# Performance work log

Measured on AMD Instinct MI355X. Metric: run time of the kernel, lower is better.

The kernel has to match this reference:

```python
import jax, jax.numpy as jnp
import numpy as np

B, S, D, H, E = 4, 4096, 1024, 16, 8
HID = 4 * D


def _ln(x, g, b, eps=1e-5):
    m = x.mean(-1, keepdims=True)
    v = ((x - m) ** 2).mean(-1, keepdims=True)
    return (x - m) / jnp.sqrt(v + eps) * g + b


def setup_inputs() -> dict:
    key = jax.random.key(0)
    ks = jax.random.split(key, 18)
    s = 0.02
    return {
        "x": jax.random.normal(ks[0], (B, S, D), jnp.float32),
        "conv_w": jax.random.normal(ks[1], (D, D, 3), jnp.float32) * s,
        "conv_b": jnp.zeros((D,), jnp.float32),
        "in_proj_w": jax.random.normal(ks[2], (3 * D, D), jnp.float32) * s,
        "in_proj_b": jnp.zeros((3 * D,), jnp.float32),
        "out_proj_w": jax.random.normal(ks[3], (D, D), jnp.float32) * s,
        "out_proj_b": jnp.zeros((D,), jnp.float32),
        "ln1_g": jnp.ones((D,), jnp.float32),
        "ln1_b": jnp.zeros((D,), jnp.float32),
        "gate_w": jax.random.normal(ks[4], (D, E), jnp.float32) * s,
        "gate_b": jnp.zeros((E,), jnp.float32),
        "w1": jax.random.normal(ks[5], (E, D, HID), jnp.float32) * s,
        "b1": jnp.zeros((E, HID), jnp.float32),
        "w2": jax.random.normal(ks[6], (E, HID, D), jnp.float32) * s,
        "b2": jnp.zeros((E, D), jnp.float32),
        "ln2_g": jnp.ones((D,), jnp.float32),
        "ln2_b": jnp.zeros((D,), jnp.float32),
    }


def reference(x, conv_w, conv_b, in_proj_w, in_proj_b, out_proj_w, out_proj_b,
              ln1_g, ln1_b, gate_w, gate_b, w1, b1, w2, b2, ln2_g, ln2_b):
    b, s, d = x.shape
    h = H
    hd = d // h
    e = w1.shape[0]
    # --- Conv1d over seq axis (kernel 3, padding 1) ---
    xc = jnp.transpose(x, (0, 2, 1))  # (B, D, S)
    xc = jax.lax.conv_general_dilated(
        xc, conv_w, (1,), [(1, 1)], dimension_numbers=("NCH", "OIH", "NCH"))
    x = jnp.transpose(xc + conv_b[None, :, None], (0, 2, 1))  # (B, S, D)
    # --- MultiheadAttention. Faithful to original: batch_first=False, so
    # axis 0 (size B) is treated as the sequence axis, axis 1 (size S) as batch.
    qkv = x @ in_proj_w.T + in_proj_b  # (B, S, 3D)
    q, k, v = jnp.split(qkv, 3, axis=-1)
    q = q.reshape(b, s, h, hd)  # l n h d (l = B, n = S)
    k = k.reshape(b, s, h, hd)
    v = v.reshape(b, s, h, hd)
    scale = 1.0 / jnp.sqrt(jnp.asarray(hd, x.dtype))
    scores = jnp.einsum("lnhd,mnhd->nhlm", q, k) * scale
    attn = jax.nn.softmax(scores, axis=-1)
    o = jnp.einsum("nhlm,mnhd->lnhd", attn, v).reshape(b, s, d)
    attn_out = o @ out_proj_w.T + out_proj_b
    x = _ln(x + attn_out, ln1_g, ln1_b)
    # --- MoE: top-2 gated FFN experts (hidden = 4*dim, ReLU) ---
    xf = x.reshape(-1, d)  # (T, D)
    t = xf.shape[0]
    probs = jax.nn.softmax(xf @ gate_w + gate_b, axis=-1)  # (T, E)
    vals, idx = jax.lax.top_k(probs, 2)
    w = vals / vals.sum(-1, keepdims=True)  # renormalized top-2 weights
    wmat = jnp.zeros((t, e), x.dtype).at[jnp.arange(t)[:, None], idx].add(w)
    y = jnp.zeros_like(xf)
    for ei in range(e):  # small fixed expert loop
        hh = jax.nn.relu(xf @ w1[ei] + b1[ei])
        y = y + wmat[:, ei:ei + 1] * (hh @ w2[ei] + b2[ei])
    moe_out = y.reshape(b, s, d)
    return _ln(x + moe_out, ln2_g, ln2_b)
```

## Files before the change

### kernel.cpp

```cpp
#include <hip/hip_runtime.h>

typedef unsigned short u16;
typedef unsigned int u32;
typedef __attribute__((ext_vector_type(8))) short bf16x8;
typedef __attribute__((ext_vector_type(8))) _Float16 f16x8;
typedef __attribute__((ext_vector_type(4))) float f32x4;

constexpr int Bq = 4, Sq = 4096, Dq = 1024, Hq = 16, Eq = 8, HIDq = 4096;
constexpr int Tq = Bq * Sq;
constexpr long TD = (long)Tq * Dq;
constexpr int PADT = 33792;
constexpr int QCN  = 1024;
constexpr int QROWS = 4 * QCN;
constexpr int ECH  = 4096;
constexpr int MAXC = 3;

constexpr long OFF_XC = 262144;
constexpr long OFF_Q  = OFF_XC + TD;
constexpr long OFF_WT = OFF_Q + (long)QROWS * 3 * Dq;
constexpr long H_B    = OFF_Q * 4;
constexpr long W1E_B  = H_B + (long)2 * ECH * HIDq;
constexpr long W2E_B  = W1E_B + (long)2 * Dq * HIDq;

__device__ __forceinline__ u32 bf1(float x) {
  u32 u = __builtin_bit_cast(u32, x);
  return (u + 0x7fffu + ((u >> 16) & 1u)) >> 16;
}
__device__ __forceinline__ u32 bfpk(float lo, float hi) {
  return bf1(lo) | (bf1(hi) << 16);
}

__device__ __forceinline__ u16 f16b(float v) {
  _Float16 h = (_Float16)v;
  return __builtin_bit_cast(u16, h);
}
__device__ __forceinline__ u32 axpk(float v) {
  _Float16 h = (_Float16)v;
  float hf = (float)h;
  u16 l = f16b((v - hf) * 4096.0f);
  return (u32)l | ((u32)__builtin_bit_cast(u16, h) << 16);
}
__device__ __forceinline__ u32 bxpk(float v) {
  _Float16 h = (_Float16)v;
  float hf = (float)h;
  u16 l = f16b((v - hf) * 4096.0f);
  return (u32)__builtin_bit_cast(u16, h) | ((u32)l << 16);
}

#define BM 128
#define BN 128

__device__ __forceinline__ void xcd_swz(int& bx, int& by) {
  const int nbx = (int)gridDim.x;
  const int nwg = nbx * (int)gridDim.y;
  int bid = (int)blockIdx.y * nbx + (int)blockIdx.x;
  bid = (bid & 7) * (nwg >> 3) + (bid >> 3);
  bx = bid % nbx;
  by = bid / nbx;
}

__device__ __forceinline__ f16x8 hi_octet(const u16* p) {
  const uint4 a = *(const uint4*)p;
  const uint4 b = *(const uint4*)(p + 1024);
  uint4 r;
  r.x = __builtin_amdgcn_perm(a.y, a.x, 0x07060302u);
  r.y = __builtin_amdgcn_perm(a.w, a.z, 0x07060302u);
  r.z = __builtin_amdgcn_perm(b.y, b.x, 0x07060302u);
  r.w = __builtin_amdgcn_perm(b.w, b.z, 0x07060302u);
  return __builtin_bit_cast(f16x8, r);
}
__device__ __forceinline__ f16x8 lo_octet(const u16* p) {
  const uint4 a = *(const uint4*)p;
  const uint4 b = *(const uint4*)(p + 1024);
  uint4 r;
  r.x = __builtin_amdgcn_perm(a.y, a.x, 0x05040100u);
  r.y = __builtin_amdgcn_perm(a.w, a.z, 0x05040100u);
  r.z = __builtin_amdgcn_perm(b.y, b.x, 0x05040100u);
  r.w = __builtin_amdgcn_perm(b.w, b.z, 0x05040100u);
  return __builtin_bit_cast(f16x8, r);
}

template <int AMODE, int EPI>
__global__ __launch_bounds__(256, 2) void gemm_h(
    const float* __restrict__ A, const u16* __restrict__ Bx,
    const float* __restrict__ bias, float* __restrict__ C,
    int Ko, int lda, int ldbN, int ldc, int nbase) {
  __shared__ __align__(16) u16 Asx[8 * 128 * 8];
  __shared__ __align__(16) u16 Bsx[8 * 128 * 8];

  const int tid = threadIdx.x;
  int sbx, sby;
  xcd_swz(sbx, sby);
  const int m0 = sby * BM;
  const int n0 = sbx * BN;

  const float* arp[2];
  int abat[2], asrow[2];
  #pragma unroll
  for (int i = 0; i < 2; i++) {
    const int f = tid + 256 * i;
    const int m = f >> 2;
    if (AMODE == 0) {
      arp[i] = A + (long)(m0 + m) * lda;
    } else if (AMODE == 1) {
      abat[i] = (m0 + m) >> 12;
      asrow[i] = (m0 + m) & 4095;
    } else {
      const int mm = m0 + m;
      const int l = mm >> 10;
      const int n = nbase + (mm & 1023);
      arp[i] = A + (long)(l * Sq + n) * lda;
    }
  }

  f32x4 acch[4][4], accx[4][4];
  #pragma unroll
  for (int i = 0; i < 4; i++)
    #pragma unroll
    for (int j = 0; j < 4; j++) {
      acch[i][j] = (f32x4)(0.f);
      accx[i][j] = (f32x4)(0.f);
    }

  const int lane = tid & 63;
  const int wave = tid >> 6;
  const int wr = wave >> 1, wc = wave & 1;
  const int q = lane >> 4, l16 = lane & 15;
  const int abase = wr * 64 + l16;
  const int bbase = wc * 64 + l16;

  for (int k0 = 0; k0 < Ko; k0 += 32) {
    #pragma unroll
    for (int i = 0; i < 2; i++) {
      const int f = tid + 256 * i;
      const int m = f >> 2, kc = f & 3;
      const int kk = k0 + kc * 8;
      float4 v0 = make_float4(0.f, 0.f, 0.f, 0.f), v1 = v0;
      if (AMODE == 1) {
        const int tap = kk >> 10, din = kk & 1023;
        const int sin = asrow[i] + tap - 1;
        if (sin >= 0 && sin < Sq) {
          const float* p = A + ((long)(abat[i] * Sq + sin) * Dq + din);
          v0 = *(const float4*)p;
          v1 = *(const float4*)(p + 4);
        }
      } else {
        v0 = *(const float4*)(arp[i] + kk);
        v1 = *(const float4*)(arp[i] + kk + 4);
      }
      uint4 wa, wb;
      wa.x = axpk(v0.x);
      wa.y = axpk(v0.y);
      wa.z = axpk(v0.z);
      wa.w = axpk(v0.w);
      wb.x = axpk(v1.x);
      wb.y = axpk(v1.y);
      wb.z = axpk(v1.z);
      wb.w = axpk(v1.w);
      *(uint4*)&Asx[((2 * kc) * 128 + m) * 8] = wa;
      *(uint4*)&Asx[((2 * kc + 1) * 128 + m) * 8] = wb;
    }
    const int kq0 = k0 >> 2;
    #pragma unroll
    for (int i = 0; i < 2; i++) {
      const int f = tid + 256 * i;
      const int kcb = f >> 7, n = f & 127;
      const u16* bp = Bx + ((long)(kq0 + 2 * kcb) * ldbN + n0 + n) * 8;
      const uint4 b0 = *(const uint4*)bp;
      const uint4 b1 = *(const uint4*)(bp + (long)ldbN * 8);
      *(uint4*)&Bsx[((2 * kcb) * 128 + n) * 8] = b0;
      *(uint4*)&Bsx[((2 * kcb + 1) * 128 + n) * 8] = b1;
    }
    __syncthreads();
    {
      f16x8 af[4], bf[4];
      #pragma unroll
      for (int mf = 0; mf < 4; mf++)
        af[mf] = hi_octet(&Asx[((2 * q) * 128 + abase + mf * 16) * 8]);
      #pragma unroll
      for (int nf = 0; nf < 4; nf++)
        bf[nf] = lo_octet(&Bsx[((2 * q) * 128 + bbase + nf * 16) * 8]);
      #pragma unroll
      for (int mf = 0; mf < 4; mf++)
        #pragma unroll
        for (int nf = 0; nf < 4; nf++)
          acch[mf][nf] = __builtin_amdgcn_mfma_f32_16x16x32_f16(
              af[mf], bf[nf], acch[mf][nf], 0, 0, 0);
      #pragma unroll
      for (int s = 0; s < 2; s++) {
        #pragma unroll
        for (int mf = 0; mf < 4; mf++)
          af[mf] =
              *(const f16x8*)&Asx[((s * 4 + q) * 128 + abase + mf * 16) * 8];
        #pragma unroll
        for (int nf = 0; nf < 4; nf++)
          bf[nf] =
              *(const f16x8*)&Bsx[((s * 4 + q) * 128 + bbase + nf * 16) * 8];
        #pragma unroll
        for (int mf = 0; mf < 4; mf++)
          #pragma unroll
          for (int nf = 0; nf < 4; nf++)
            accx[mf][nf] = __builtin_amdgcn_mfma_f32_16x16x32_f16(
                af[mf], bf[nf], accx[mf][nf], 0, 0, 0);
      }
    }
    __syncthreads();
  }

  float bcol[4];
  #pragma unroll
  for (int nf = 0; nf < 4; nf++) bcol[nf] = bias[n0 + wc * 64 + nf * 16 + l16];
  #pragma unroll
  for (int mf = 0; mf < 4; mf++) {
    #pragma unroll
    for (int reg = 0; reg < 4; reg++) {
      const int row = wr * 64 + mf * 16 + q * 4 + reg;
      float* crow = C + (long)(m0 + row) * ldc;
      #pragma unroll
      for (int nf = 0; nf < 4; nf++) {
        const int col = n0 + wc * 64 + nf * 16 + l16;
        float v = acch[mf][nf][reg] + accx[mf][nf][reg] * (1.0f / 4096.0f) +
                  bcol[nf];
        if (EPI == 2) v += crow[col];
        crow[col] = v;
      }
    }
  }
}

template <int AMODE, int EPI>
__global__ __launch_bounds__(256) void gemm_b(
    const void* __restrict__ Av, const u16* __restrict__ Bmf,
    const float* __restrict__ bias, void* __restrict__ Cv,
    int K, int lda, int ldbN, int ldc,
    const int* __restrict__ list, const float* __restrict__ wslot,
    const int* __restrict__ offsp, const int* __restrict__ counts,
    float* __restrict__ moe, int eidx, int cbase) {
  __shared__ __align__(16) u16 As[8 * 128 * 8];
  __shared__ __align__(16) u16 Bs[8 * 128 * 8];

  const int tid = threadIdx.x;
  int sbx, sby;
  xcd_swz(sbx, sby);
  const int rel = cbase + sby * BM;
  const int cnt = counts[eidx];
  const int padded = ((cnt + 127) >> 7) << 7;
  if (rel >= padded) return;
  const int count_e = cnt;
  const int lr0 = rel;
  const int r0 = offsp[eidx] + rel;
  const int n0 = sbx * BN;
  const int mrow0 = sby * BM;

  const float* aptr[4];
  const u16* aptr6[4];
  bool aval[4];
  #pragma unroll
  for (int i = 0; i < 4; i++) {
    const int f = tid + 256 * i;
    const int m = f >> 3;
    aval[i] = true;
    if (AMODE == 5) {
      const int lr = lr0 + m;
      aval[i] = (lr < count_e);
      const int tok = aval[i] ? list[r0 + m] : 0;
      aptr[i] = (const float*)Av + (long)tok * lda;
    } else {
      aptr6[i] = (const u16*)Av + (long)(mrow0 + m) * lda;
    }
  }

  f32x4 acc[4][4];
  #pragma unroll
  for (int i = 0; i < 4; i++)
    #pragma unroll
    for (int j = 0; j < 4; j++) acc[i][j] = (f32x4)(0.f);

  const int lane = tid & 63;
  const int wave = tid >> 6;
  const int wr = wave >> 1, wc = wave & 1;
  const int q = lane >> 4, l16 = lane & 15;

  for (int k0 = 0; k0 < K; k0 += 64) {
    #pragma unroll
    for (int i = 0; i < 4; i++) {
      const int f = tid + 256 * i;
      const int m = f >> 3, kc = f & 7;
      const int kk = k0 + kc * 8;
      uint4 w;
      if (AMODE == 6) {
        w = *(const uint4*)(aptr6[i] + kk);
      } else {
        float4 v0 = make_float4(0.f, 0.f, 0.f, 0.f), v1 = v0;
        if (aval[i]) {
          v0 = *(const float4*)(aptr[i] + kk);
          v1 = *(const float4*)(aptr[i] + kk + 4);
        }
        w.x = bfpk(v0.x, v0.y);
        w.y = bfpk(v0.z, v0.w);
        w.z = bfpk(v1.x, v1.y);
        w.w = bfpk(v1.z, v1.w);
      }
      *(uint4*)&As[(kc * 128 + m) * 8] = w;
    }
    const int kc0 = k0 >> 3;
    #pragma unroll
    for (int i = 0; i < 4; i++) {
      const int f = tid + 256 * i;
      const int kcb = f >> 7, n = f & 127;
      const uint4 wb =
          *(const uint4*)(Bmf + ((long)(kc0 + kcb) * ldbN + n0 + n) * 8);
      *(uint4*)&Bs[(kcb * 128 + n) * 8] = wb;
    }
    __syncthreads();
    #pragma unroll
    for (int s = 0; s < 2; s++) {
      bf16x8 af[4], bfr[4];
      #pragma unroll
      for (int mf = 0; mf < 4; mf++)
        af[mf] = *(const bf16x8*)
            &As[((s * 4 + q) * 128 + wr * 64 + mf * 16 + l16) * 8];
      #pragma unroll
      for (int nf = 0; nf < 4; nf++)
        bfr[nf] = *(const bf16x8*)
            &Bs[((s * 4 + q) * 128 + wc * 64 + nf * 16 + l16) * 8];
      #pragma unroll
      for (int mf = 0; mf < 4; mf++)
        #pragma unroll
        for (int nf = 0; nf < 4; nf++)
          acc[mf][nf] = __builtin_amdgcn_mfma_f32_16x16x32_bf16(
              af[mf], bfr[nf], acc[mf][nf], 0, 0, 0);
    }
    __syncthreads();
  }

  float bcol[4];
  #pragma unroll
  for (int nf = 0; nf < 4; nf++) bcol[nf] = bias[n0 + wc * 64 + nf * 16 + l16];
  #pragma unroll
  for (int mf = 0; mf < 4; mf++) {
    #pragma unroll
    for (int reg = 0; reg < 4; reg++) {
      const int row = wr * 64 + mf * 16 + q * 4 + reg;
      if (lr0 + row >= count_e) continue;
      int tok = 0;
      float wgt = 0.f;
      if (EPI == 3) {
        tok = list[r0 + row];
        wgt = wslot[r0 + row];
      }
      #pragma unroll
      for (int nf = 0; nf < 4; nf++) {
        float v = acc[mf][nf][reg] + bcol[nf];
        const int col = n0 + wc * 64 + nf * 16 + l16;
        if (EPI == 3) {
          float* mp = moe + (long)tok * Dq + col;
          *mp = *mp + wgt * v;
        } else {
          v = fmaxf(v, 0.f);
          ((u16*)Cv)[(long)(mrow0 + row) * ldc + col] = (u16)bf1(v);
        }
      }
    }
  }
}

__global__ __launch_bounds__(256) void wsplit_conv(const float* __restrict__ cw,
                                                   u16* __restrict__ dst) {
  const int n = blockIdx.x * 256 + threadIdx.x;
  const int kc = blockIdx.y;
  uint4 w;
  u32* wp = (u32*)&w;
  #pragma unroll
  for (int j = 0; j < 4; j++) {
    const int k = kc * 4 + j;
    const int tap = k >> 10, din = k & 1023;
    wp[j] = bxpk(cw[(long)n * 3072 + din * 3 + tap]);
  }
  *(uint4*)(dst + ((long)kc * 1024 + n) * 8) = w;
}

__global__ __launch_bounds__(256) void wsplit_nk(const float* __restrict__ src,
                                                 u16* __restrict__ dst, int N,
                                                 int K) {
  const int n = blockIdx.x * 256 + threadIdx.x;
  const int kc = blockIdx.y;
  const float4 v = *(const float4*)(src + (long)n * K + kc * 4);
  uint4 w;
  w.x = bxpk(v.x);
  w.y = bxpk(v.y);
  w.z = bxpk(v.z);
  w.w = bxpk(v.w);
  *(uint4*)(dst + ((long)kc * N + n) * 8) = w;
}

__global__ __launch_bounds__(256) void kn2b_k(const float* __restrict__ src,
                                              u16* __restrict__ dst, int N) {
  const int n = blockIdx.x * 256 + threadIdx.x;
  const int kc = blockIdx.y;
  float v[8];
  #pragma unroll
  for (int j = 0; j < 8; j++) v[j] = src[(long)(kc * 8 + j) * N + n];
  uint4 w;
  w.x = bfpk(v[0], v[1]);
  w.y = bfpk(v[2], v[3]);
  w.z = bfpk(v[4], v[5]);
  w.w = bfpk(v[6], v[7]);
  *(uint4*)(dst + ((long)kc * N + n) * 8) = w;
}

__global__ __launch_bounds__(256) void attn_k(const float* __restrict__ qc,
                                              float* __restrict__ o, int nbase) {
  const int wid = blockIdx.x * 4 + (threadIdx.x >> 6);
  const int lane = threadIdx.x & 63;
  const int h = wid & 15;
  const int nl = wid >> 4;
  float q[4], k[4], v[4];
  #pragma unroll
  for (int l = 0; l < 4; l++) {
    const long base = (long)(l * QCN + nl) * 3072 + h * 64 + lane;
    q[l] = qc[base];
    k[l] = qc[base + Dq];
    v[l] = qc[base + 2 * Dq];
  }
  float sc[4][4];
  #pragma unroll
  for (int l = 0; l < 4; l++)
    #pragma unroll
    for (int m = 0; m < 4; m++) sc[l][m] = q[l] * k[m];
  #pragma unroll
  for (int off = 32; off >= 1; off >>= 1)
    #pragma unroll
    for (int l = 0; l < 4; l++)
      #pragma unroll
      for (int m = 0; m < 4; m++) sc[l][m] += __shfl_xor(sc[l][m], off, 64);
  float p[4][4];
  #pragma unroll
  for (int l = 0; l < 4; l++) {
    float s0[4], mx = -1e30f;
    #pragma unroll
    for (int m = 0; m < 4; m++) { s0[m] = sc[l][m] * 0.125f; mx = fmaxf(mx, s0[m]); }
    float sum = 0.f;
    #pragma unroll
    for (int m = 0; m < 4; m++) { p[l][m] = __expf(s0[m] - mx); sum += p[l][m]; }
    const float inv = 1.0f / sum;
    #pragma unroll
    for (int m = 0; m < 4; m++) p[l][m] *= inv;
  }
  #pragma unroll
  for (int l = 0; l < 4; l++) {
    float ov = 0.f;
    #pragma unroll
    for (int m = 0; m < 4; m++) ov = fmaf(p[l][m], v[m], ov);
    o[(long)(l * Sq + nbase + nl) * Dq + h * 64 + lane] = ov;
  }
}

__device__ __forceinline__ float block_sum256(float v, float* sbuf) {
  #pragma unroll
  for (int off = 32; off >= 1; off >>= 1) v += __shfl_xor(v, off, 64);
  const int w = threadIdx.x >> 6;
  __syncthreads();
  if ((threadIdx.x & 63) == 0) sbuf[w] = v;
  __syncthreads();
  return sbuf[0] + sbuf[1] + sbuf[2] + sbuf[3];
}

__device__ __forceinline__ void ln_core(const float xv[4], const float* g,
                                        const float* bb, float* outp, long base,
                                        float* sbuf) {
  const float tot = block_sum256(xv[0] + xv[1] + xv[2] + xv[3], sbuf);
  const float mean = tot * (1.0f / 1024.0f);
  const float d0 = xv[0] - mean, d1 = xv[1] - mean, d2 = xv[2] - mean,
              d3 = xv[3] - mean;
  const float var =
      block_sum256(d0 * d0 + d1 * d1 + d2 * d2 + d3 * d3, sbuf) * (1.0f / 1024.0f);
  const float inv = 1.0f / sqrtf(var + 1e-5f);
  const int c = threadIdx.x * 4;
  const float4 gg = *(const float4*)(g + c);
  const float4 bv = *(const float4*)(bb + c);
  float4 r;
  r.x = d0 * inv * gg.x + bv.x;
  r.y = d1 * inv * gg.y + bv.y;
  r.z = d2 * inv * gg.z + bv.z;
  r.w = d3 * inv * gg.w + bv.w;
  *(float4*)(outp + base) = r;
}

__global__ __launch_bounds__(256) void ln1_k(const float* __restrict__ xc,
                                             const float* __restrict__ g,
                                             const float* __restrict__ bb,
                                             float* __restrict__ outp) {
  __shared__ float sbuf[4];
  const long base = (long)blockIdx.x * Dq + threadIdx.x * 4;
  const float4 a = *(const float4*)(xc + base);
  const float xv[4] = {a.x, a.y, a.z, a.w};
  ln_core(xv, g, bb, outp, base, sbuf);
}

__global__ __launch_bounds__(256) void ln2_k(const float* __restrict__ x1,
                                             const float* __restrict__ moe,
                                             const float* __restrict__ g,
                                             const float* __restrict__ bb,
                                             float* __restrict__ outp) {
  __shared__ float sbuf[4];
  const long base = (long)blockIdx.x * Dq + threadIdx.x * 4;
  const float4 a = *(const float4*)(x1 + base);
  const float4 m = *(const float4*)(moe + base);
  const float xv[4] = {a.x + m.x, a.y + m.y, a.z + m.z, a.w + m.w};
  ln_core(xv, g, bb, outp, base, sbuf);
}

__global__ __launch_bounds__(256) void gate_k(const float* __restrict__ x1,
                                              const float* __restrict__ gw,
                                              const float* __restrict__ gb,
                                              int* __restrict__ e01,
                                              float* __restrict__ w01) {
  const int t = blockIdx.x * 4 + (threadIdx.x >> 6);
  const int lane = threadIdx.x & 63;
  const float* xr = x1 + (long)t * Dq;
  float acc[8];
  #pragma unroll
  for (int e = 0; e < 8; e++) acc[e] = 0.f;
  #pragma unroll
  for (int j = 0; j < 16; j++) {
    const int d = lane + 64 * j;
    const float xv = xr[d];
    const float4 g0 = *(const float4*)(gw + d * 8);
    const float4 g1 = *(const float4*)(gw + d * 8 + 4);
    acc[0] = fmaf(xv, g0.x, acc[0]);
    acc[1] = fmaf(xv, g0.y, acc[1]);
    acc[2] = fmaf(xv, g0.z, acc[2]);
    acc[3] = fmaf(xv, g0.w, acc[3]);
    acc[4] = fmaf(xv, g1.x, acc[4]);
    acc[5] = fmaf(xv, g1.y, acc[5]);
    acc[6] = fmaf(xv, g1.z, acc[6]);
    acc[7] = fmaf(xv, g1.w, acc[7]);
  }
  #pragma unroll
  for (int off = 32; off >= 1; off >>= 1)
    #pragma unroll
    for (int e = 0; e < 8; e++) acc[e] += __shfl_xor(acc[e], off, 64);
  if (lane == 0) {
    float mx = -1e30f;
    #pragma unroll
    for (int e = 0; e < 8; e++) { acc[e] += gb[e]; mx = fmaxf(mx, acc[e]); }
    float Z = 0.f, p[8];
    #pragma unroll
    for (int e = 0; e < 8; e++) { p[e] = __expf(acc[e] - mx); Z += p[e]; }
    const float invZ = 1.0f / Z;
    float b0 = -1.f, b1 = -1.f;
    int i0 = 0, i1 = 0;
    #pragma unroll
    for (int e = 0; e < 8; e++) {
      const float pe = p[e] * invZ;
      if (pe > b0) { b1 = b0; i1 = i0; b0 = pe; i0 = e; }
      else if (pe > b1) { b1 = pe; i1 = e; }
    }
    const float s = b0 + b1;
    e01[2 * t] = i0;
    e01[2 * t + 1] = i1;
    w01[2 * t] = b0 / s;
    w01[2 * t + 1] = b1 / s;
  }
}

__global__ void zero_k(int* p) {
  if (threadIdx.x < 16) p[threadIdx.x] = 0;
}

__global__ __launch_bounds__(256) void zerof_k(float* __restrict__ p) {
  const long i = ((long)blockIdx.x * 256 + threadIdx.x) * 4;
  *(float4*)(p + i) = make_float4(0.f, 0.f, 0.f, 0.f);
}

__global__ __launch_bounds__(256) void count_k(const int* __restrict__ e01,
                                               int* __restrict__ counts) {
  __shared__ int lc[8];
  const int tid = threadIdx.x;
  if (tid < 8) lc[tid] = 0;
  __syncthreads();
  const int t = blockIdx.x * 256 + tid;
  atomicAdd(&lc[e01[2 * t]], 1);
  atomicAdd(&lc[e01[2 * t + 1]], 1);
  __syncthreads();
  if (tid < 8) atomicAdd(&counts[tid], lc[tid]);
}

__global__ void offs_k(const int* __restrict__ counts, int* __restrict__ offsp) {
  if (threadIdx.x == 0) {
    int a = 0;
    for (int e = 0; e < 8; e++) {
      offsp[e] = a;
      a += ((counts[e] + 127) >> 7) << 7;
    }
    offsp[8] = a;
  }
}

__global__ __launch_bounds__(256) void scatter_k(
    const int* __restrict__ e01, const float* __restrict__ w01,
    int* __restrict__ cursor, const int* __restrict__ offsp,
    int* __restrict__ list, float* __restrict__ wslot) {
  __shared__ int lc[8];
  __shared__ int gbase[8];
  const int tid = threadIdx.x;
  if (tid < 8) lc[tid] = 0;
  __syncthreads();
  const int t = blockIdx.x * 256 + tid;
  const int e0 = e01[2 * t], e1 = e01[2 * t + 1];
  const int p0 = atomicAdd(&lc[e0], 1);
  const int p1 = atomicAdd(&lc[e1], 1);
  __syncthreads();
  if (tid < 8) gbase[tid] = atomicAdd(&cursor[tid], lc[tid]);
  __syncthreads();
  const int s0 = offsp[e0] + gbase[e0] + p0;
  const int s1 = offsp[e1] + gbase[e1] + p1;
  list[s0] = t;
  list[s1] = t;
  wslot[s0] = w01[2 * t];
  wslot[s1] = w01[2 * t + 1];
}

extern "C" void kernel_launch(void* const* d_in, const int* in_sizes, int n_in,
                              void* d_out, int out_size, void* d_ws,
                              size_t ws_size, hipStream_t stream) {
  const float* x          = (const float*)d_in[0];
  const float* conv_w     = (const float*)d_in[1];
  const float* conv_b     = (const float*)d_in[2];
  const float* in_proj_w  = (const float*)d_in[3];
  const float* in_proj_b  = (const float*)d_in[4];
  const float* out_proj_w = (const float*)d_in[5];
  const float* out_proj_b = (const float*)d_in[6];
  const float* ln1_g      = (const float*)d_in[7];
  const float* ln1_b      = (const float*)d_in[8];
  const float* gate_w     = (const float*)d_in[9];
  const float* gate_b     = (const float*)d_in[10];
  const float* w1         = (const float*)d_in[11];
  const float* b1         = (const float*)d_in[12];
  const float* w2         = (const float*)d_in[13];
  const float* b2         = (const float*)d_in[14];
  const float* ln2_g      = (const float*)d_in[15];
  const float* ln2_b      = (const float*)d_in[16];

  float* ws = (float*)d_ws;
  char* wsb = (char*)d_ws;
  int* si      = (int*)ws;
  int* counts  = si;
  int* cursor  = si + 8;
  int* offsp   = si + 16;
  int* e01     = si + 32;
  float* w01   = (float*)(si + 32 + 2 * Tq);
  int* list    = si + 32 + 4 * Tq;
  float* wslot = (float*)(list + PADT);

  float* xc   = ws + OFF_XC;
  float* moe  = ws + OFF_XC;
  float* qc   = ws + OFF_Q;
  u16* wtx    = (u16*)(ws + OFF_WT);
  u16* h      = (u16*)(wsb + H_B);
  u16* w1be   = (u16*)(wsb + W1E_B);
  u16* w2be   = (u16*)(wsb + W2E_B);
  float* o    = (float*)d_out;
  float* x1   = (float*)d_out;
  float* out  = (float*)d_out;

  zero_k<<<1, 64, 0, stream>>>(counts);
  wsplit_conv<<<dim3(4, 768), 256, 0, stream>>>(conv_w, wtx);
  gemm_h<1, 0><<<dim3(Dq / BN, Tq / BM), 256, 0, stream>>>(
      x, wtx, conv_b, xc, 3 * Dq, Dq, Dq, Dq, 0);
  wsplit_nk<<<dim3(12, 256), 256, 0, stream>>>(in_proj_w, wtx, 3 * Dq, Dq);
  for (int c = 0; c < Sq / QCN; c++) {
    gemm_h<4, 0><<<dim3(3 * Dq / BN, QROWS / BM), 256, 0, stream>>>(
        xc, wtx, in_proj_b, qc, Dq, Dq, 3 * Dq, 3 * Dq, c * QCN);
    attn_k<<<(QCN * Hq) / 4, 256, 0, stream>>>(qc, o, c * QCN);
  }
  wsplit_nk<<<dim3(4, 256), 256, 0, stream>>>(out_proj_w, wtx, Dq, Dq);
  gemm_h<0, 2><<<dim3(Dq / BN, Tq / BM), 256, 0, stream>>>(
      o, wtx, out_proj_b, xc, Dq, Dq, Dq, Dq, 0);
  ln1_k<<<Tq, 256, 0, stream>>>(xc, ln1_g, ln1_b, x1);
  zerof_k<<<Tq, 256, 0, stream>>>(moe);
  gate_k<<<Tq / 4, 256, 0, stream>>>(x1, gate_w, gate_b, e01, w01);
  count_k<<<Tq / 256, 256, 0, stream>>>(e01, counts);
  offs_k<<<1, 64, 0, stream>>>(counts, offsp);
  scatter_k<<<Tq / 256, 256, 0, stream>>>(e01, w01, cursor, offsp, list, wslot);
  for (int e = 0; e < Eq; e++) {
    kn2b_k<<<dim3(HIDq / 256, Dq / 8), 256, 0, stream>>>(
        w1 + (long)e * Dq * HIDq, w1be, HIDq);
    kn2b_k<<<dim3(Dq / 256, HIDq / 8), 256, 0, stream>>>(
        w2 + (long)e * HIDq * Dq, w2be, Dq);
    for (int c = 0; c < MAXC; c++) {
      gemm_b<5, 1><<<dim3(HIDq / BN, ECH / BM), 256, 0, stream>>>(
          x1, w1be, b1 + (long)e * HIDq, h, Dq, Dq, HIDq, HIDq,
          list, wslot, offsp, counts, nullptr, e, c * ECH);
      gemm_b<6, 3><<<dim3(Dq / BN, ECH / BM), 256, 0, stream>>>(
          h, w2be, b2 + (long)e * Dq, nullptr, HIDq, HIDq, Dq, Dq,
          list, wslot, offsp, counts, moe, e, c * ECH);
    }
  }
  ln2_k<<<Tq, 256, 0, stream>>>(x1, moe, ln2_g, ln2_b, out);
}
```

Before: 3.649 ms.

## Double-buffer B tiles via direct global-to-LDS loads and prefetch A in registers

```diff
diff --git a/kernel.cpp b/kernel.cpp
--- a/kernel.cpp
+++ b/kernel.cpp
@@ -49,6 +49,11 @@
 
 #define BM 128
 #define BN 128
+
+#define GLL16(SRC, DST)                                                \
+  __builtin_amdgcn_global_load_lds(                                    \
+      (const __attribute__((address_space(1))) void*)(SRC),            \
+      (__attribute__((address_space(3))) void*)(DST), 16, 0, 0)
 
 __device__ __forceinline__ void xcd_swz(int& bx, int& by) {
   const int nbx = (int)gridDim.x;
@@ -86,7 +91,7 @@
     const float* __restrict__ bias, float* __restrict__ C,
     int Ko, int lda, int ldbN, int ldc, int nbase) {
   __shared__ __align__(16) u16 Asx[8 * 128 * 8];
-  __shared__ __align__(16) u16 Bsx[8 * 128 * 8];
+  __shared__ __align__(16) u16 Bsx[2][8 * 128 * 8];
 
   const int tid = threadIdx.x;
   int sbx, sby;
@@ -129,57 +134,79 @@
   const int abase = wr * 64 + l16;
   const int bbase = wc * 64 + l16;
 
-  for (int k0 = 0; k0 < Ko; k0 += 32) {
+  auto loadA = [&](int k0, float4 v0[2], float4 v1[2]) {
     #pragma unroll
     for (int i = 0; i < 2; i++) {
       const int f = tid + 256 * i;
-      const int m = f >> 2, kc = f & 3;
+      const int kc = f & 3;
       const int kk = k0 + kc * 8;
-      float4 v0 = make_float4(0.f, 0.f, 0.f, 0.f), v1 = v0;
+      float4 a0 = make_float4(0.f, 0.f, 0.f, 0.f), a1 = a0;
       if (AMODE == 1) {
         const int tap = kk >> 10, din = kk & 1023;
         const int sin = asrow[i] + tap - 1;
         if (sin >= 0 && sin < Sq) {
           const float* p = A + ((long)(abat[i] * Sq + sin) * Dq + din);
-          v0 = *(const float4*)p;
-          v1 = *(const float4*)(p + 4);
+          a0 = *(const float4*)p;
+          a1 = *(const float4*)(p + 4);
         }
       } else {
-        v0 = *(const float4*)(arp[i] + kk);
-        v1 = *(const float4*)(arp[i] + kk + 4);
+        a0 = *(const float4*)(arp[i] + kk);
+        a1 = *(const float4*)(arp[i] + kk + 4);
       }
-      uint4 wa, wb;
-      wa.x = axpk(v0.x);
-      wa.y = axpk(v0.y);
-      wa.z = axpk(v0.z);
-      wa.w = axpk(v0.w);
-      wb.x = axpk(v1.x);
-      wb.y = axpk(v1.y);
-      wb.z = axpk(v1.z);
-      wb.w = axpk(v1.w);
-      *(uint4*)&Asx[((2 * kc) * 128 + m) * 8] = wa;
-      *(uint4*)&Asx[((2 * kc + 1) * 128 + m) * 8] = wb;
-    }
+      v0[i] = a0;
+      v1[i] = a1;
+    }
+  };
+
+  auto issueB = [&](int k0, int buf) {
     const int kq0 = k0 >> 2;
     #pragma unroll
     for (int i = 0; i < 2; i++) {
       const int f = tid + 256 * i;
       const int kcb = f >> 7, n = f & 127;
       const u16* bp = Bx + ((long)(kq0 + 2 * kcb) * ldbN + n0 + n) * 8;
-      const uint4 b0 = *(const uint4*)bp;
-      const uint4 b1 = *(const uint4*)(bp + (long)ldbN * 8);
-      *(uint4*)&Bsx[((2 * kcb) * 128 + n) * 8] = b0;
-      *(uint4*)&Bsx[((2 * kcb + 1) * 128 + n) * 8] = b1;
+      GLL16(bp, &Bsx[buf][((2 * kcb) * 128 + n) * 8]);
+      GLL16(bp + (long)ldbN * 8, &Bsx[buf][((2 * kcb + 1) * 128 + n) * 8]);
+    }
+  };
+
+  float4 pv0[2], pv1[2];
+  loadA(0, pv0, pv1);
+  issueB(0, 0);
+
+  int cur = 0;
+  for (int k0 = 0; k0 < Ko; k0 += 32) {
+    #pragma unroll
+    for (int i = 0; i < 2; i++) {
+      const int f = tid + 256 * i;
+      const int m = f >> 2, kc = f & 3;
+      uint4 wa, wb;
+      wa.x = axpk(pv0[i].x);
+      wa.y = axpk(pv0[i].y);
+      wa.z = axpk(pv0[i].z);
+      wa.w = axpk(pv0[i].w);
+      wb.x = axpk(pv1[i].x);
+      wb.y = axpk(pv1[i].y);
+      wb.z = axpk(pv1[i].z);
+      wb.w = axpk(pv1[i].w);
+      *(uint4*)&Asx[((2 * kc) * 128 + m) * 8] = wa;
+      *(uint4*)&Asx[((2 * kc + 1) * 128 + m) * 8] = wb;
     }
     __syncthreads();
+    const bool more = (k0 + 32 < Ko);
+    if (more) {
+      loadA(k0 + 32, pv0, pv1);
+      issueB(k0 + 32, cur ^ 1);
+    }
     {
+      const u16* Bc = Bsx[cur];
       f16x8 af[4], bf[4];
       #pragma unroll
       for (int mf = 0; mf < 4; mf++)
         af[mf] = hi_octet(&Asx[((2 * q) * 128 + abase + mf * 16) * 8]);
       #pragma unroll
       for (int nf = 0; nf < 4; nf++)
-        bf[nf] = lo_octet(&Bsx[((2 * q) * 128 + bbase + nf * 16) * 8]);
+        bf[nf] = lo_octet(&Bc[((2 * q) * 128 + bbase + nf * 16) * 8]);
       #pragma unroll
       for (int mf = 0; mf < 4; mf++)
         #pragma unroll
@@ -195,7 +222,7 @@
         #pragma unroll
         for (int nf = 0; nf < 4; nf++)
           bf[nf] =
-              *(const f16x8*)&Bsx[((s * 4 + q) * 128 + bbase + nf * 16) * 8];
+              *(const f16x8*)&Bc[((s * 4 + q) * 128 + bbase + nf * 16) * 8];
         #pragma unroll
         for (int mf = 0; mf < 4; mf++)
           #pragma unroll
@@ -205,6 +232,7 @@
       }
     }
     __syncthreads();
+    cur ^= 1;
   }
 
   float bcol[4];
@@ -237,7 +265,7 @@
     const int* __restrict__ offsp, const int* __restrict__ counts,
     float* __restrict__ moe, int eidx, int cbase) {
   __shared__ __align__(16) u16 As[8 * 128 * 8];
-  __shared__ __align__(16) u16 Bs[8 * 128 * 8];
+  __shared__ __align__(16) u16 Bs[2][8 * 128 * 8];
 
   const int tid = threadIdx.x;
   int sbx, sby;
@@ -280,6 +308,20 @@
   const int wave = tid >> 6;
   const int wr = wave >> 1, wc = wave & 1;
   const int q = lane >> 4, l16 = lane & 15;
+
+  auto issueB = [&](int k0, int buf) {
+    const int kc0 = k0 >> 3;
+    #pragma unroll
+    for (int i = 0; i < 4; i++) {
+      const int f = tid + 256 * i;
+      const int kcb = f >> 7, n = f & 127;
+      const u16* bp = Bmf + ((long)(kc0 + kcb) * ldbN + n0 + n) * 8;
+      GLL16(bp, &Bs[buf][(kcb * 128 + n) * 8]);
+    }
+  };
+
+  issueB(0, 0);
+  int cur = 0;
 
   for (int k0 = 0; k0 < K; k0 += 64) {
     #pragma unroll
@@ -303,35 +345,31 @@
       }
       *(uint4*)&As[(kc * 128 + m) * 8] = w;
     }
-    const int kc0 = k0 >> 3;
-    #pragma unroll
-    for (int i = 0; i < 4; i++) {
-      const int f = tid + 256 * i;
-      const int kcb = f >> 7, n = f & 127;
-      const uint4 wb =
-          *(const uint4*)(Bmf + ((long)(kc0 + kcb) * ldbN + n0 + n) * 8);
-      *(uint4*)&Bs[(kcb * 128 + n) * 8] = wb;
-    }
     __syncthreads();
-    #pragma unroll
-    for (int s = 0; s < 2; s++) {
-      bf16x8 af[4], bfr[4];
+    if (k0 + 64 < K) issueB(k0 + 64, cur ^ 1);
+    {
+      const u16* Bc = Bs[cur];
       #pragma unroll
-      for (int mf = 0; mf < 4; mf++)
-        af[mf] = *(const bf16x8*)
-            &As[((s * 4 + q) * 128 + wr * 64 + mf * 16 + l16) * 8];
-      #pragma unroll
-      for (int nf = 0; nf < 4; nf++)
-        bfr[nf] = *(const bf16x8*)
-            &Bs[((s * 4 + q) * 128 + wc * 64 + nf * 16 + l16) * 8];
-      #pragma unroll
-      for (int mf = 0; mf < 4; mf++)
+      for (int s = 0; s < 2; s++) {
+        bf16x8 af[4], bfr[4];
+        #pragma unroll
+        for (int mf = 0; mf < 4; mf++)
+          af[mf] = *(const bf16x8*)
+              &As[((s * 4 + q) * 128 + wr * 64 + mf * 16 + l16) * 8];
         #pragma unroll
         for (int nf = 0; nf < 4; nf++)
-          acc[mf][nf] = __builtin_amdgcn_mfma_f32_16x16x32_bf16(
-              af[mf], bfr[nf], acc[mf][nf], 0, 0, 0);
+          bfr[nf] = *(const bf16x8*)
+              &Bc[((s * 4 + q) * 128 + wc * 64 + nf * 16 + l16) * 8];
+        #pragma unroll
+        for (int mf = 0; mf < 4; mf++)
+          #pragma unroll
+          for (int nf = 0; nf < 4; nf++)
+            acc[mf][nf] = __builtin_amdgcn_mfma_f32_16x16x32_bf16(
+                af[mf], bfr[nf], acc[mf][nf], 0, 0, 0);
+      }
     }
     __syncthreads();
+    cur ^= 1;
   }
 
   float bcol[4];
```

Measured after the change: 4.211 ms. +15.4%, slower.
